# Performance work log

Hardware: AMD Instinct MI355X
Metric: run time of the kernel (lower is better)

## Reference

```python
import jax, jax.numpy as jnp
import numpy as np

B, SQ, SKV, D = 4, 4096, 4096, 64

def setup_inputs() -> dict:
    key = jax.random.key(0)
    kq, kk, kv = jax.random.split(key, 3)
    return {
        "q": jax.random.normal(kq, (B, SQ, D), dtype=jnp.float32),
        "k": jax.random.normal(kk, (B, SKV, D), dtype=jnp.float32),
        "v": jax.random.normal(kv, (B, SKV, D), dtype=jnp.float32),
        "inv_scale_factor": 8,
        "is_training": 0,
    }

def reference(q, k, v, inv_scale_factor, is_training):
    # qk = q @ k^T, divided by inv_scale_factor, softmax over keys
    scores = jnp.einsum("bqd,bkd->bqk", q, k) / inv_scale_factor  # [B,SQ,SKV]
    attn = jax.nn.softmax(scores, axis=-1)
    # dropout is deterministic identity (eval mode, is_training=0)
    out = jnp.einsum("bqk,bkd->bqd", attn, v)  # [B,SQ,D]
    # should_apply_residual before loop
    out = out + q
    # 3-iteration chain: residual add + normalization add (+2q), dropout (identity),
    # sigmoid, clamp(0,1)
    for _ in range(3):
        out = out + 2.0 * q
        out = jax.nn.sigmoid(out)
        out = jnp.clip(out, 0.0, 1.0)
    return out
```

## Files before the change

### kernel.cpp

```cpp
#include <hip/hip_runtime.h>

#define SQd 4096
#define SKVd 4096
#define DDIM 64
#define BQ 64
#define BK 32
#define NG 8
#define NTILES (SKVd / BK)
#define TPG (NTILES / NG)
#define FRAG_ELEMS 512
#define TILE_ELEMS (4 * FRAG_ELEMS)
#define KWS_ELEMS (4 * NTILES * TILE_ELEMS)

typedef __bf16 bf16x8 __attribute__((ext_vector_type(8)));
typedef float floatx4 __attribute__((ext_vector_type(4)));

struct CombS {
    float Ored[BQ][4][68];
    float Lred[BQ][NG];
};

__global__ __launch_bounds__(256)
void prepack_kernel(const float* __restrict__ k, const float* __restrict__ v,
                    __bf16* __restrict__ ws)
{
    const int t = blockIdx.x * 256 + threadIdx.x;
    const int id   = t & (KWS_ELEMS / 8 - 1);
    const int lane = id & 63;
    const int l16  = lane & 15;
    const int quad = lane >> 4;
    const int h    = (id >> 6) & 3;
    const int tile = (id >> 8) & (NTILES - 1);
    const int b    = id >> 15;
    bf16x8 o;
    if (t < KWS_ELEMS / 8) {
        const int row = tile * BK + (h >> 1) * 16 + l16;
        const int col = (h & 1) * 32 + quad * 8;
        const float* p = k + ((size_t)b * SKVd + row) * DDIM + col;
        const float4 a0 = *(const float4*)p;
        const float4 a1 = *(const float4*)(p + 4);
        o[0] = (__bf16)a0.x; o[1] = (__bf16)a0.y; o[2] = (__bf16)a0.z; o[3] = (__bf16)a0.w;
        o[4] = (__bf16)a1.x; o[5] = (__bf16)a1.y; o[6] = (__bf16)a1.z; o[7] = (__bf16)a1.w;
        ((bf16x8*)ws)[id] = o;
    } else {
        const int col = h * 16 + l16;
        #pragma unroll
        for (int j = 0; j < 8; ++j) {
            const int key = tile * BK + 16 * (j >> 2) + quad * 4 + (j & 3);
            o[j] = (__bf16)v[((size_t)b * SKVd + key) * DDIM + col];
        }
        ((bf16x8*)(ws + KWS_ELEMS))[id] = o;
    }
}

__global__ __launch_bounds__(512, 2)
void fattn_kernel(const float* __restrict__ q, const int* __restrict__ isf_p,
                  const __bf16* __restrict__ kws, const __bf16* __restrict__ vws,
                  float* __restrict__ out)
{
    __shared__ __align__(16) CombS C;

    const int tid  = threadIdx.x;
    const int g    = tid >> 6;
    const int lane = tid & 63;
    const int l16  = lane & 15;
    const int quad = lane >> 4;

    const int bidx  = blockIdx.x;
    const int b     = (bidx & 7) >> 1;
    const int qtile = ((bidx & 1) << 5) | (bidx >> 3);

    const float scale = 1.0f / (float)(*isf_p);

    bf16x8 qf[4][2];
    #pragma unroll
    for (int qg = 0; qg < 4; ++qg) {
        const int qrow = qtile * BQ + qg * 16 + l16;
        const float* qp = q + ((size_t)b * SQd + qrow) * DDIM + quad * 8;
        #pragma unroll
        for (int dh = 0; dh < 2; ++dh) {
            const float4 a0 = *(const float4*)(qp + dh * 32);
            const float4 a1 = *(const float4*)(qp + dh * 32 + 4);
            qf[qg][dh][0] = (__bf16)(a0.x * scale); qf[qg][dh][1] = (__bf16)(a0.y * scale);
            qf[qg][dh][2] = (__bf16)(a0.z * scale); qf[qg][dh][3] = (__bf16)(a0.w * scale);
            qf[qg][dh][4] = (__bf16)(a1.x * scale); qf[qg][dh][5] = (__bf16)(a1.y * scale);
            qf[qg][dh][6] = (__bf16)(a1.z * scale); qf[qg][dh][7] = (__bf16)(a1.w * scale);
        }
    }

    const __bf16* kg = kws + ((size_t)b * NTILES + g * TPG) * TILE_ELEMS + lane * 8;
    const __bf16* vg = vws + ((size_t)b * NTILES + g * TPG) * TILE_ELEMS + lane * 8;

    floatx4 o[4][4];
    float l_acc[4];
    #pragma unroll
    for (int qg = 0; qg < 4; ++qg) {
        l_acc[qg] = 0.0f;
        #pragma unroll
        for (int nb = 0; nb < 4; ++nb)
            #pragma unroll
            for (int r = 0; r < 4; ++r) o[qg][nb][r] = 0.0f;
    }

    const floatx4 zf = {0.0f, 0.0f, 0.0f, 0.0f};

    auto step = [&](bf16x8* kc, bf16x8* vc, bf16x8* kn, bf16x8* vn, int itn) {
        const size_t noff = (size_t)itn * TILE_ELEMS;
        #pragma unroll
        for (int h = 0; h < 4; ++h)
            kn[h] = *(const bf16x8*)(kg + noff + h * FRAG_ELEMS);
        #pragma unroll
        for (int h = 0; h < 4; ++h)
            vn[h] = *(const bf16x8*)(vg + noff + h * FRAG_ELEMS);

        bf16x8 pf[4];
        #pragma unroll
        for (int qg = 0; qg < 4; ++qg) {
            floatx4 s0 = zf, s1 = zf;
            s0 = __builtin_amdgcn_mfma_f32_16x16x32_bf16(kc[0], qf[qg][0], s0, 0, 0, 0);
            s0 = __builtin_amdgcn_mfma_f32_16x16x32_bf16(kc[1], qf[qg][1], s0, 0, 0, 0);
            s1 = __builtin_amdgcn_mfma_f32_16x16x32_bf16(kc[2], qf[qg][0], s1, 0, 0, 0);
            s1 = __builtin_amdgcn_mfma_f32_16x16x32_bf16(kc[3], qf[qg][1], s1, 0, 0, 0);
            float lsum = 0.0f;
            #pragma unroll
            for (int r = 0; r < 4; ++r) {
                const float p0 = __expf(s0[r]);
                const float p1 = __expf(s1[r]);
                pf[qg][r]     = (__bf16)p0;
                pf[qg][4 + r] = (__bf16)p1;
                lsum += p0 + p1;
            }
            l_acc[qg] += lsum;
        }
        #pragma unroll
        for (int nb = 0; nb < 4; ++nb)
            #pragma unroll
            for (int qg = 0; qg < 4; ++qg)
                o[qg][nb] = __builtin_amdgcn_mfma_f32_16x16x32_bf16(pf[qg], vc[nb], o[qg][nb], 0, 0, 0);
    };

    bf16x8 k0[4], v0[4], k1[4], v1[4];
    #pragma unroll
    for (int h = 0; h < 4; ++h) {
        k0[h] = *(const bf16x8*)(kg + h * FRAG_ELEMS);
        v0[h] = *(const bf16x8*)(vg + h * FRAG_ELEMS);
    }
    for (int t = 0; t < TPG / 2; ++t) {
        step(k0, v0, k1, v1, 2 * t + 1);
        step(k1, v1, k0, v0, (2 * t + 2 < TPG) ? 2 * t + 2 : TPG - 1);
    }

    #pragma unroll
    for (int qg = 0; qg < 4; ++qg) {
        l_acc[qg] += __shfl_xor(l_acc[qg], 16);
        l_acc[qg] += __shfl_xor(l_acc[qg], 32);
    }
    if (quad == 0) {
        #pragma unroll
        for (int qg = 0; qg < 4; ++qg)
            C.Lred[qg * 16 + l16][g] = l_acc[qg];
    }

    if (g < 4) {
        #pragma unroll
        for (int qg = 0; qg < 4; ++qg)
            #pragma unroll
            for (int nb = 0; nb < 4; ++nb)
                #pragma unroll
                for (int r = 0; r < 4; ++r)
                    C.Ored[qg * 16 + quad * 4 + r][g][nb * 16 + l16] = o[qg][nb][r];
    }
    __syncthreads();
    if (g >= 4) {
        #pragma unroll
        for (int qg = 0; qg < 4; ++qg)
            #pragma unroll
            for (int nb = 0; nb < 4; ++nb)
                #pragma unroll
                for (int r = 0; r < 4; ++r)
                    C.Ored[qg * 16 + quad * 4 + r][g - 4][nb * 16 + l16] += o[qg][nb][r];
    }
    __syncthreads();

    {
        const int row = tid >> 3;
        const int d8  = (tid & 7) * 8;
        float l = 0.0f;
        #pragma unroll
        for (int gg = 0; gg < NG; ++gg) l += C.Lred[row][gg];
        const float rl = 1.0f / l;
        #pragma unroll
        for (int half = 0; half < 2; ++half) {
            const int d4 = d8 + half * 4;
            float xs[4] = {0.f, 0.f, 0.f, 0.f};
            #pragma unroll
            for (int s = 0; s < 4; ++s) {
                const float4 t4 = *(const float4*)&C.Ored[row][s][d4];
                xs[0] += t4.x; xs[1] += t4.y; xs[2] += t4.z; xs[3] += t4.w;
            }
            const size_t idx = ((size_t)b * SQd + qtile * BQ + row) * DDIM + d4;
            const float4 q4 = *(const float4*)(q + idx);
            const float qs[4] = {q4.x, q4.y, q4.z, q4.w};
            #pragma unroll
            for (int c = 0; c < 4; ++c) {
                float x = xs[c] * rl + qs[c];
                #pragma unroll
                for (int itc = 0; itc < 3; ++itc) {
                    x = x + 2.0f * qs[c];
                    x = 1.0f / (1.0f + __expf(-x));
                    x = fminf(fmaxf(x, 0.0f), 1.0f);
                }
                xs[c] = x;
            }
            const float4 r4 = {xs[0], xs[1], xs[2], xs[3]};
            *(float4*)(out + idx) = r4;
        }
    }
}

extern "C" void kernel_launch(void* const* d_in, const int* in_sizes, int n_in,
                              void* d_out, int out_size, void* d_ws, size_t ws_size,
                              hipStream_t stream) {
    const float* q = (const float*)d_in[0];
    const float* k = (const float*)d_in[1];
    const float* v = (const float*)d_in[2];
    const int* isf = (const int*)d_in[3];
    float* out = (float*)d_out;
    __bf16* ws = (__bf16*)d_ws;

    prepack_kernel<<<dim3(1024), dim3(256), 0, stream>>>(k, v, ws);

    const int nblocks = 4 * (SQd / BQ);
    fattn_kernel<<<dim3(nblocks), dim3(512), 0, stream>>>(
        q, isf, ws, ws + KWS_ELEMS, out);
}
```

Measured before the change: 92.63 us.

## Stage prepack through LDS, deepen K prefetch, fold log2e into exp2

The prepack kernel now loads each 32-key tile of K and V coalesced into shared memory and then scatters it into MFMA fragment order, replacing strided per-element V reads from global memory. The attention loop is fully unrolled with a three-deep K buffer and a two-deep V buffer, so K is prefetched two tiles ahead. The softmax scale now includes log2(e), which lets the exponent use the hardware exp2 instruction directly. Full unrolling of the 16 tiles per group and the extra buffers raise register pressure under the two-blocks-per-CU launch bound.

```diff
diff --git a/kernel.cpp b/kernel.cpp
--- a/kernel.cpp
+++ b/kernel.cpp
@@ -13,6 +13,7 @@
 #define KWS_ELEMS (4 * NTILES * TILE_ELEMS)
 
 typedef __bf16 bf16x8 __attribute__((ext_vector_type(8)));
+typedef __bf16 bf16x4 __attribute__((ext_vector_type(4)));
 typedef float floatx4 __attribute__((ext_vector_type(4)));
 
 struct CombS {
@@ -24,33 +25,44 @@
 void prepack_kernel(const float* __restrict__ k, const float* __restrict__ v,
                     __bf16* __restrict__ ws)
 {
-    const int t = blockIdx.x * 256 + threadIdx.x;
-    const int id   = t & (KWS_ELEMS / 8 - 1);
-    const int lane = id & 63;
+    __shared__ __align__(16) __bf16 Kt[BK][72];
+    __shared__ __align__(16) __bf16 Vt[BK][72];
+
+    const int blk  = blockIdx.x;
+    const int b    = blk >> 7;
+    const int tile = blk & (NTILES - 1);
+    const int tid  = threadIdx.x;
+
+    const size_t base = ((size_t)b * SKVd + tile * BK) * DDIM;
+    #pragma unroll
+    for (int p = 0; p < 2; ++p) {
+        const int e   = tid * 4 + p * 1024;
+        const int row = e >> 6, col = e & 63;
+        const float4 k4 = *(const float4*)(k + base + (size_t)row * DDIM + col);
+        bf16x4 kk4; kk4[0] = (__bf16)k4.x; kk4[1] = (__bf16)k4.y;
+        kk4[2] = (__bf16)k4.z; kk4[3] = (__bf16)k4.w;
+        *(bf16x4*)&Kt[row][col] = kk4;
+        const float4 v4 = *(const float4*)(v + base + (size_t)row * DDIM + col);
+        bf16x4 vv4; vv4[0] = (__bf16)v4.x; vv4[1] = (__bf16)v4.y;
+        vv4[2] = (__bf16)v4.z; vv4[3] = (__bf16)v4.w;
+        *(bf16x4*)&Vt[row][col] = vv4;
+    }
+    __syncthreads();
+
+    const int lane = tid & 63;
     const int l16  = lane & 15;
     const int quad = lane >> 4;
-    const int h    = (id >> 6) & 3;
-    const int tile = (id >> 8) & (NTILES - 1);
-    const int b    = id >> 15;
-    bf16x8 o;
-    if (t < KWS_ELEMS / 8) {
-        const int row = tile * BK + (h >> 1) * 16 + l16;
-        const int col = (h & 1) * 32 + quad * 8;
-        const float* p = k + ((size_t)b * SKVd + row) * DDIM + col;
-        const float4 a0 = *(const float4*)p;
-        const float4 a1 = *(const float4*)(p + 4);
-        o[0] = (__bf16)a0.x; o[1] = (__bf16)a0.y; o[2] = (__bf16)a0.z; o[3] = (__bf16)a0.w;
-        o[4] = (__bf16)a1.x; o[5] = (__bf16)a1.y; o[6] = (__bf16)a1.z; o[7] = (__bf16)a1.w;
-        ((bf16x8*)ws)[id] = o;
-    } else {
-        const int col = h * 16 + l16;
-        #pragma unroll
-        for (int j = 0; j < 8; ++j) {
-            const int key = tile * BK + 16 * (j >> 2) + quad * 4 + (j & 3);
-            o[j] = (__bf16)v[((size_t)b * SKVd + key) * DDIM + col];
-        }
-        ((bf16x8*)(ws + KWS_ELEMS))[id] = o;
-    }
+    const int f    = tid >> 6;
+
+    const bf16x8 kf = *(const bf16x8*)&Kt[(f >> 1) * 16 + l16][(f & 1) * 32 + quad * 8];
+    bf16x8 vf;
+    #pragma unroll
+    for (int j = 0; j < 8; ++j)
+        vf[j] = Vt[16 * (j >> 2) + quad * 4 + (j & 3)][f * 16 + l16];
+
+    const size_t obase = ((size_t)b * NTILES + tile) * TILE_ELEMS + (size_t)f * FRAG_ELEMS + lane * 8;
+    *(bf16x8*)(ws + obase) = kf;
+    *(bf16x8*)(ws + KWS_ELEMS + obase) = vf;
 }
 
 __global__ __launch_bounds__(512, 2)
@@ -70,7 +82,7 @@
     const int b     = (bidx & 7) >> 1;
     const int qtile = ((bidx & 1) << 5) | (bidx >> 3);
 
-    const float scale = 1.0f / (float)(*isf_p);
+    const float scale = 1.44269504088896340736f / (float)(*isf_p);
 
     bf16x8 qf[4][2];
     #pragma unroll
@@ -101,17 +113,33 @@
             #pragma unroll
             for (int r = 0; r < 4; ++r) o[qg][nb][r] = 0.0f;
     }
-
     const floatx4 zf = {0.0f, 0.0f, 0.0f, 0.0f};
 
-    auto step = [&](bf16x8* kc, bf16x8* vc, bf16x8* kn, bf16x8* vn, int itn) {
-        const size_t noff = (size_t)itn * TILE_ELEMS;
-        #pragma unroll
-        for (int h = 0; h < 4; ++h)
-            kn[h] = *(const bf16x8*)(kg + noff + h * FRAG_ELEMS);
-        #pragma unroll
-        for (int h = 0; h < 4; ++h)
-            vn[h] = *(const bf16x8*)(vg + noff + h * FRAG_ELEMS);
+    bf16x8 kb[3][4], vb[2][4];
+    #pragma unroll
+    for (int h = 0; h < 4; ++h) {
+        kb[0][h] = *(const bf16x8*)(kg + h * FRAG_ELEMS);
+        kb[1][h] = *(const bf16x8*)(kg + TILE_ELEMS + h * FRAG_ELEMS);
+        vb[0][h] = *(const bf16x8*)(vg + h * FRAG_ELEMS);
+    }
+
+    #pragma unroll
+    for (int t = 0; t < TPG; ++t) {
+        if (t + 2 < TPG) {
+            const size_t koff = (size_t)(t + 2) * TILE_ELEMS;
+            #pragma unroll
+            for (int h = 0; h < 4; ++h)
+                kb[(t + 2) % 3][h] = *(const bf16x8*)(kg + koff + h * FRAG_ELEMS);
+        }
+        if (t + 1 < TPG) {
+            const size_t voff = (size_t)(t + 1) * TILE_ELEMS;
+            #pragma unroll
+            for (int h = 0; h < 4; ++h)
+                vb[(t + 1) % 2][h] = *(const bf16x8*)(vg + voff + h * FRAG_ELEMS);
+        }
+
+        const bf16x8* kc = kb[t % 3];
+        const bf16x8* vc = vb[t % 2];
 
         bf16x8 pf[4];
         #pragma unroll
@@ -124,8 +152,8 @@
             float lsum = 0.0f;
             #pragma unroll
             for (int r = 0; r < 4; ++r) {
-                const float p0 = __expf(s0[r]);
-                const float p1 = __expf(s1[r]);
+                const float p0 = __builtin_amdgcn_exp2f(s0[r]);
+                const float p1 = __builtin_amdgcn_exp2f(s1[r]);
                 pf[qg][r]     = (__bf16)p0;
                 pf[qg][4 + r] = (__bf16)p1;
                 lsum += p0 + p1;
@@ -137,17 +165,6 @@
             #pragma unroll
             for (int qg = 0; qg < 4; ++qg)
                 o[qg][nb] = __builtin_amdgcn_mfma_f32_16x16x32_bf16(pf[qg], vc[nb], o[qg][nb], 0, 0, 0);
-    };
-
-    bf16x8 k0[4], v0[4], k1[4], v1[4];
-    #pragma unroll
-    for (int h = 0; h < 4; ++h) {
-        k0[h] = *(const bf16x8*)(kg + h * FRAG_ELEMS);
-        v0[h] = *(const bf16x8*)(vg + h * FRAG_ELEMS);
-    }
-    for (int t = 0; t < TPG / 2; ++t) {
-        step(k0, v0, k1, v1, 2 * t + 1);
-        step(k1, v1, k0, v0, (2 * t + 2 < TPG) ? 2 * t + 2 : TPG - 1);
     }
 
     #pragma unroll
@@ -228,7 +245,7 @@
     float* out = (float*)d_out;
     __bf16* ws = (__bf16*)d_ws;
 
-    prepack_kernel<<<dim3(1024), dim3(256), 0, stream>>>(k, v, ws);
+    prepack_kernel<<<dim3(4 * NTILES), dim3(256), 0, stream>>>(k, v, ws);
 
     const int nblocks = 4 * (SQd / BQ);
     fattn_kernel<<<dim3(nblocks), dim3(512), 0, stream>>>(
```

New measurement: 91.80 us. About the same (-0.9%).
